# Optimization experiments

Hardware: AMD Instinct MI355X
Metric: run time of the kernel (lower is better)

## Reference

```python
import jax, jax.numpy as jnp
import numpy as np

BATCH, TOK, DIM, OUT = 4, 2048, 4096, 4096
E, R, TOP_K = 8, 16, 2
SCALING = 16.0 / R  # lora_alpha / r


def setup_inputs() -> dict:
    key = jax.random.key(0)
    ks = jax.random.split(key, 6)
    return {
        "x": jax.random.normal(ks[0], (BATCH, TOK, DIM), dtype=jnp.float32),
        "W_base": jax.random.normal(ks[1], (OUT, DIM), dtype=jnp.float32) / np.sqrt(DIM),
        "b_base": jax.random.normal(ks[2], (OUT,), dtype=jnp.float32) * 0.01,
        "W_gate": jax.random.normal(ks[3], (E, DIM), dtype=jnp.float32) * 0.01,
        "A": jax.random.normal(ks[4], (E, R, DIM), dtype=jnp.float32) / np.sqrt(DIM),
        "B": jax.random.normal(ks[5], (OUT, OUT // OUT * R * 0 + R), dtype=jnp.float32)[None].repeat(E, 0) * 0.0 + jax.random.normal(ks[5], (E, OUT, R), dtype=jnp.float32) * 0.02,
    }


def reference(x, W_base, b_base, W_gate, A, B):
    # Base frozen linear: [B,N,D] @ [D,O] -> [B,N,O]
    result = jnp.einsum("bnd,od->bno", x, W_base) + b_base
    # Gating
    logits = jnp.einsum("bnd,ed->bne", x, W_gate)
    probs = jax.nn.softmax(logits.astype(jnp.float32), axis=-1)  # fp32 softmax
    top_p, top_i = jax.lax.top_k(probs, TOP_K)  # [B,N,K]
    top_p = top_p / jnp.sum(top_p, axis=-1, keepdims=True)  # top_k > 1 branch
    top_p = top_p.astype(x.dtype)
    # Scatter top-k probs back to dense [B,N,E] routing weights
    route_w = jnp.sum(jax.nn.one_hot(top_i, E, dtype=x.dtype) * top_p[..., None], axis=-2)
    # Per-expert LoRA: down-project all tokens for all experts (r is small),
    # weight by routing, then up-project and sum over experts.
    h = jnp.einsum("bnd,erd->bner", x, A)          # [B,N,E,r]
    hw = h * route_w[..., None]                      # mask/combine weighting
    delta = jnp.einsum("bner,eor->bno", hw, B)      # [B,N,O]
    return result + delta * SCALING
```

## Files before the change

### kernel.cpp

```cpp
#include <hip/hip_runtime.h>
#include <hip/hip_bf16.h>
#include <cstdint>

#define TOKENS 8192
#define DIM_   4096
#define OUTD   4096
#define NE     8
#define NR     16
#define LORA_COLS (NE*NR)
#define KCAT  (DIM_ + LORA_COLS)
#define NTILES (KCAT/64)

typedef __attribute__((ext_vector_type(8))) short short8;
typedef __attribute__((ext_vector_type(4))) float f32x4;

__device__ __forceinline__ unsigned short f2bf(float f) {
  union { float f; unsigned u; } v; v.f = f;
  unsigned r = v.u + 0x7FFFu + ((v.u >> 16) & 1u);
  return (unsigned short)(r >> 16);
}

__device__ __forceinline__ void load_lds16(const void* g, void* l) {
  auto gp = reinterpret_cast<const __attribute__((address_space(1))) unsigned int*>(
      reinterpret_cast<uintptr_t>(g));
  auto lp = reinterpret_cast<__attribute__((address_space(3))) unsigned int*>(
      reinterpret_cast<uintptr_t>(l));
  __builtin_amdgcn_global_load_lds(gp, lp, 16, 0, 0);
}

#define BAR() asm volatile("s_barrier" ::: "memory")
#define LGKM0() do { asm volatile("s_waitcnt lgkmcnt(0)" ::: "memory"); \
                     __builtin_amdgcn_sched_barrier(0); } while (0)
#define VMW(N) asm volatile("s_waitcnt vmcnt(" #N ")" ::: "memory")

__global__ __launch_bounds__(256) void conv_w_kernel(
    const float* __restrict__ W, const float* __restrict__ Bm,
    const float* __restrict__ Am, unsigned short* __restrict__ Wcat,
    unsigned short* __restrict__ Acat, float scaling) {
  int b = blockIdx.x, tid = threadIdx.x;
  if (b < OUTD) {
    const float4* src = (const float4*)(W + (size_t)b * DIM_);
    unsigned short* dst = Wcat + (size_t)b * KCAT;
#pragma unroll
    for (int j = 0; j < DIM_ / 1024; ++j) {
      float4 v = src[j * 256 + tid];
      ushort4 o; o.x = f2bf(v.x); o.y = f2bf(v.y); o.z = f2bf(v.z); o.w = f2bf(v.w);
      *(ushort4*)(dst + (size_t)(j * 256 + tid) * 4) = o;
    }
    if (tid < LORA_COLS) {
      int e = tid >> 4, r = tid & 15;
      dst[DIM_ + tid] = f2bf(scaling * Bm[((size_t)e * OUTD + b) * NR + r]);
    }
  } else {
    int i = b - OUTD;
    const float4* src = (const float4*)(Am + (size_t)i * DIM_);
    unsigned short* dst = Acat + (size_t)i * DIM_;
#pragma unroll
    for (int j = 0; j < DIM_ / 1024; ++j) {
      float4 v = src[j * 256 + tid];
      ushort4 o; o.x = f2bf(v.x); o.y = f2bf(v.y); o.z = f2bf(v.z); o.w = f2bf(v.w);
      *(ushort4*)(dst + (size_t)(j * 256 + tid) * 4) = o;
    }
  }
}

__global__ __launch_bounds__(256) void prep_x_kernel(
    const float* __restrict__ x, const float* __restrict__ Wg,
    unsigned short* __restrict__ Xcat, int* __restrict__ ridx,
    float* __restrict__ rw) {
  __shared__ float red[32 * 257];
  __shared__ float lg[32];
  int tid = threadIdx.x;
  int t0 = blockIdx.x * 4;
  float acc[4][8];
#pragma unroll
  for (int ti = 0; ti < 4; ++ti)
#pragma unroll
    for (int e = 0; e < 8; ++e) acc[ti][e] = 0.f;
  const float4* x4 = (const float4*)x;
  const float4* wg4 = (const float4*)Wg;
#pragma unroll
  for (int j = 0; j < 4; ++j) {
    int dpos = j * 256 + tid;
    float4 wg[8];
#pragma unroll
    for (int e = 0; e < 8; ++e) wg[e] = wg4[e * 1024 + dpos];
#pragma unroll
    for (int ti = 0; ti < 4; ++ti) {
      float4 v = x4[(size_t)(t0 + ti) * 1024 + dpos];
      ushort4 o; o.x = f2bf(v.x); o.y = f2bf(v.y); o.z = f2bf(v.z); o.w = f2bf(v.w);
      *(ushort4*)&Xcat[(size_t)(t0 + ti) * KCAT + (size_t)dpos * 4] = o;
#pragma unroll
      for (int e = 0; e < 8; ++e)
        acc[ti][e] += v.x * wg[e].x + v.y * wg[e].y + v.z * wg[e].z + v.w * wg[e].w;
    }
  }
#pragma unroll
  for (int p = 0; p < 32; ++p) red[p * 257 + tid] = acc[p >> 3][p & 7];
  __syncthreads();
  {
    int p = tid >> 3, part = tid & 7;
    float s = 0.f;
#pragma unroll
    for (int i = 0; i < 32; ++i) s += red[p * 257 + part * 32 + i];
    s += __shfl_xor(s, 1);
    s += __shfl_xor(s, 2);
    s += __shfl_xor(s, 4);
    if (part == 0) lg[p] = s;
  }
  __syncthreads();
  if (tid < 4) {
    float l[8];
#pragma unroll
    for (int e = 0; e < 8; ++e) l[e] = lg[tid * 8 + e];
    int i0 = 0; float m0 = l[0];
#pragma unroll
    for (int e = 1; e < 8; ++e) if (l[e] > m0) { m0 = l[e]; i0 = e; }
    int i1 = -1; float m1 = -3.4e38f;
#pragma unroll
    for (int e = 0; e < 8; ++e) if (e != i0 && l[e] > m1) { m1 = l[e]; i1 = e; }
    float w0 = 1.0f / (1.0f + expf(m1 - m0));
    int t = t0 + tid;
    ridx[t * 2] = i0; ridx[t * 2 + 1] = i1;
    rw[t * 2] = w0;  rw[t * 2 + 1] = 1.0f - w0;
  }
}

template <int MODE>
__global__ __launch_bounds__(256) void gemm_kernel(
    const unsigned short* __restrict__ Aop, const unsigned short* __restrict__ Bop,
    float* __restrict__ Cout, unsigned short* __restrict__ CoutBf,
    const float* __restrict__ bias, const int* __restrict__ ridx,
    const float* __restrict__ rw,
    int M, int N, int K, int lda, int ldb, int ldc) {
  __shared__ __align__(16) unsigned short lsA[128 * 32];
  __shared__ __align__(16) unsigned short lsB[128 * 32];
  int tid = threadIdx.x;
  int lane = tid & 63, wave = tid >> 6;
  int wm = wave >> 1, wn = wave & 1;
  int row0 = blockIdx.x * 128, col0 = blockIdx.y * 128;

  f32x4 acc[4][4];
#pragma unroll
  for (int a = 0; a < 4; ++a)
#pragma unroll
    for (int b = 0; b < 4; ++b) acc[a][b] = (f32x4){0.f, 0.f, 0.f, 0.f};

  int lrow = lane >> 2;
  int lcol = (lane & 3) << 3;
  int fr = lane & 15, fk = (lane >> 4) << 3;

  const unsigned short* gA0 = Aop + (size_t)(row0 + wave * 32 + lrow) * lda + lcol;
  const unsigned short* gA1 = Aop + (size_t)(row0 + wave * 32 + 16 + lrow) * lda + lcol;
  const unsigned short* gB0 = Bop + (size_t)(col0 + wave * 32 + lrow) * ldb + lcol;
  const unsigned short* gB1 = Bop + (size_t)(col0 + wave * 32 + 16 + lrow) * ldb + lcol;

  for (int k0 = 0; k0 < K; k0 += 32) {
    load_lds16(gA0 + k0, lsA + wave * 1024);
    load_lds16(gA1 + k0, lsA + wave * 1024 + 512);
    load_lds16(gB0 + k0, lsB + wave * 1024);
    load_lds16(gB1 + k0, lsB + wave * 1024 + 512);
    __syncthreads();
    short8 af[4], bfr[4];
#pragma unroll
    for (int mi = 0; mi < 4; ++mi)
      af[mi] = *(const short8*)&lsA[(wm * 64 + mi * 16 + fr) * 32 + fk];
#pragma unroll
    for (int ni = 0; ni < 4; ++ni)
      bfr[ni] = *(const short8*)&lsB[(wn * 64 + ni * 16 + fr) * 32 + fk];
#pragma unroll
    for (int mi = 0; mi < 4; ++mi)
#pragma unroll
      for (int ni = 0; ni < 4; ++ni)
        acc[mi][ni] = __builtin_amdgcn_mfma_f32_16x16x32_bf16(af[mi], bfr[ni], acc[mi][ni], 0, 0, 0);
    __syncthreads();
  }

  int fg = lane >> 4;
  if (MODE == 0) {
#pragma unroll
    for (int ni = 0; ni < 4; ++ni) {
      int col = col0 + wn * 64 + ni * 16 + fr;
      float bv = bias[col];
#pragma unroll
      for (int mi = 0; mi < 4; ++mi)
#pragma unroll
        for (int j = 0; j < 4; ++j) {
          int row = row0 + wm * 64 + mi * 16 + fg * 4 + j;
          Cout[(size_t)row * ldc + col] = acc[mi][ni][j] + bv;
        }
    }
  } else {
#pragma unroll
    for (int mi = 0; mi < 4; ++mi)
#pragma unroll
      for (int j = 0; j < 4; ++j) {
        int row = row0 + wm * 64 + mi * 16 + fg * 4 + j;
        int i0 = ridx[row * 2], i1 = ridx[row * 2 + 1];
        float w0 = rw[row * 2], w1 = rw[row * 2 + 1];
#pragma unroll
        for (int ni = 0; ni < 4; ++ni) {
          int col = wn * 64 + ni * 16 + fr;
          int e = col >> 4;
          float w = (e == i0) ? w0 : ((e == i1) ? w1 : 0.f);
          CoutBf[(size_t)row * ldc + col] = f2bf(w * acc[mi][ni][j]);
        }
      }
  }
}

#define RD_A4(dst, base, ks, mi0) do { \
  dst[0] = *(const short8*)((base) + (((mi0)+0)*2+(ks))*1024); \
  dst[1] = *(const short8*)((base) + (((mi0)+1)*2+(ks))*1024); \
  dst[2] = *(const short8*)((base) + (((mi0)+2)*2+(ks))*1024); \
  dst[3] = *(const short8*)((base) + (((mi0)+3)*2+(ks))*1024); } while (0)
#define RD_B4(dst, base, ks) do { \
  dst[0] = *(const short8*)((base) + 0*2048 + (ks)*1024); \
  dst[1] = *(const short8*)((base) + 1*2048 + (ks)*1024); \
  dst[2] = *(const short8*)((base) + 2*2048 + (ks)*1024); \
  dst[3] = *(const short8*)((base) + 3*2048 + (ks)*1024); } while (0)
#define MFMA_BLK(a4, b4, m0) do { \
  __builtin_amdgcn_s_setprio(1); \
  _Pragma("unroll") \
  for (int mi = 0; mi < 4; ++mi) { \
    _Pragma("unroll") \
    for (int ni = 0; ni < 4; ++ni) { \
      acc[(m0)+mi][ni] = __builtin_amdgcn_mfma_f32_16x16x32_bf16( \
          a4[mi], b4[ni], acc[(m0)+mi][ni], 0, 0, 0); } } \
  __builtin_amdgcn_s_setprio(0); } while (0)
#define STAGE(srcp, kofs, dst) do { \
  load_lds16((srcp) + (kofs), (dst)); \
  load_lds16((srcp) + (kofs) + 32, (dst) + 1024); } while (0)

__global__ __launch_bounds__(512, 2) void gemm256_kernel(
    const unsigned short* __restrict__ Aop,
    const unsigned short* __restrict__ Bop,
    float* __restrict__ Cout, const float* __restrict__ bias) {
  extern __shared__ char lds[];
  const int tid = threadIdx.x;
  const int lane = tid & 63, wave = tid >> 6;
  const int wm = wave >> 2, wn = wave & 3;
  const int fr = lane & 15, kg = lane >> 4;

  const int bid = blockIdx.x;
  const int swz = (bid & 7) * 64 + (bid >> 3);
  const int mt = swz >> 4, nt = swz & 15;
  const int row0 = mt * 256, col0 = nt * 256;

  const int srow = lane >> 2;
  const int scol = ((lane & 3) * 8) ^ (((lane >> 5) & 1) * 16);
  const unsigned short* sA0 = Aop + (size_t)(row0 +       wave * 16 + srow) * KCAT + scol;
  const unsigned short* sA1 = Aop + (size_t)(row0 + 128 + wave * 16 + srow) * KCAT + scol;
  const unsigned short* sB0 = Bop + (size_t)(col0 +       wave * 16 + srow) * KCAT + scol;
  const unsigned short* sB1 = Bop + (size_t)(col0 + 128 + wave * 16 + srow) * KCAT + scol;

  char* dA0b0 = lds +      0 + wave * 2048;
  char* dA1b0 = lds +  16384 + wave * 2048;
  char* dB0b0 = lds +  32768 + wave * 2048;
  char* dB1b0 = lds +  49152 + wave * 2048;
  char* dA0b1 = dA0b0 + 65536;
  char* dA1b1 = dA1b0 + 65536;
  char* dB0b1 = dB0b0 + 65536;
  char* dB1b1 = dB1b0 + 65536;

  const int swzo = (kg * 16) ^ ((fr >> 3) << 5);
  const char* rdA0 = lds + wm * 16384 + fr * 64 + swzo;
  const char* rdA1 = rdA0 + 65536;
  const char* rdB0 = lds + 32768 + (wn >> 1) * 16384 + (wn & 1) * 8192 + fr * 64 + swzo;
  const char* rdB1 = rdB0 + 65536;

  f32x4 acc[8][4];
#pragma unroll
  for (int a = 0; a < 8; ++a)
#pragma unroll
    for (int b = 0; b < 4; ++b) acc[a][b] = (f32x4){0.f, 0.f, 0.f, 0.f};

  STAGE(sA0, 0, dA0b0); STAGE(sA1, 0, dA1b0);
  STAGE(sB0, 0, dB0b0); STAGE(sB1, 0, dB1b0);
  STAGE(sB0, 64, dB0b1); STAGE(sA0, 64, dA0b1);
  VMW(4);
  BAR();

  for (int i = 0; i < NTILES / 2 - 1; ++i) {
    const int k1 = (2 * i + 1) * 64, k2 = k1 + 64, k3 = k1 + 128;
    short8 aL[4], aH[4], a1L[4], a1H[4], b0f[4], b1f[4];
    RD_A4(aL, rdA0, 0, 0); RD_B4(b0f, rdB0, 0);
    STAGE(sB1, k1, dB1b1);
    BAR(); LGKM0();
    MFMA_BLK(aL, b0f, 0);
    BAR();
    RD_A4(aH, rdA0, 0, 4); RD_B4(b1f, rdB0, 1);
    STAGE(sA1, k1, dA1b1);
    BAR(); LGKM0();
    MFMA_BLK(aH, b0f, 4);
    BAR();
    RD_A4(a1L, rdA0, 1, 0); RD_A4(a1H, rdA0, 1, 4);
    STAGE(sB0, k2, dB0b0);
    BAR(); LGKM0();
    MFMA_BLK(a1L, b1f, 0);
    BAR();
    STAGE(sA0, k2, dA0b0);
    BAR();
    MFMA_BLK(a1H, b1f, 4);
    VMW(4);
    BAR();
    RD_A4(aL, rdA1, 0, 0); RD_B4(b0f, rdB1, 0);
    STAGE(sB1, k2, dB1b0);
    BAR(); LGKM0();
    MFMA_BLK(aL, b0f, 0);
    BAR();
    RD_A4(aH, rdA1, 0, 4); RD_B4(b1f, rdB1, 1);
    STAGE(sA1, k2, dA1b0);
    BAR(); LGKM0();
    MFMA_BLK(aH, b0f, 4);
    BAR();
    RD_A4(a1L, rdA1, 1, 0); RD_A4(a1H, rdA1, 1, 4);
    STAGE(sB0, k3, dB0b1);
    BAR(); LGKM0();
    MFMA_BLK(a1L, b1f, 0);
    BAR();
    STAGE(sA0, k3, dA0b1);
    BAR();
    MFMA_BLK(a1H, b1f, 4);
    VMW(4);
    BAR();
  }

  {
    const int k65 = 65 * 64;
    short8 aL[4], aH[4], a1L[4], a1H[4], b0f[4], b1f[4];
    RD_A4(aL, rdA0, 0, 0); RD_B4(b0f, rdB0, 0);
    STAGE(sB1, k65, dB1b1);
    BAR(); LGKM0();
    MFMA_BLK(aL, b0f, 0);
    BAR();
    RD_A4(aH, rdA0, 0, 4); RD_B4(b1f, rdB0, 1);
    STAGE(sA1, k65, dA1b1);
    BAR(); LGKM0();
    MFMA_BLK(aH, b0f, 4);
    BAR();
    RD_A4(a1L, rdA0, 1, 0); RD_A4(a1H, rdA0, 1, 4);
    BAR(); LGKM0();
    MFMA_BLK(a1L, b1f, 0);
    BAR();
    MFMA_BLK(a1H, b1f, 4);
    VMW(0);
    BAR();
    RD_A4(aL, rdA1, 0, 0); RD_B4(b0f, rdB1, 0); RD_A4(aH, rdA1, 0, 4);
    LGKM0();
    MFMA_BLK(aL, b0f, 0);
    MFMA_BLK(aH, b0f, 4);
    RD_A4(a1L, rdA1, 1, 0); RD_B4(b1f, rdB1, 1); RD_A4(a1H, rdA1, 1, 4);
    LGKM0();
    MFMA_BLK(a1L, b1f, 0);
    MFMA_BLK(a1H, b1f, 4);
  }

#pragma unroll
  for (int ni = 0; ni < 4; ++ni) {
    int col = col0 + wn * 64 + ni * 16 + fr;
    float bv = bias[col];
#pragma unroll
    for (int mi = 0; mi < 8; ++mi)
#pragma unroll
      for (int j = 0; j < 4; ++j) {
        int row = row0 + wm * 128 + mi * 16 + kg * 4 + j;
        Cout[(size_t)row * OUTD + col] = acc[mi][ni][j] + bv;
      }
  }
}

extern "C" void kernel_launch(void* const* d_in, const int* in_sizes, int n_in,
                              void* d_out, int out_size, void* d_ws, size_t ws_size,
                              hipStream_t stream) {
  const float* x  = (const float*)d_in[0];
  const float* Wb = (const float*)d_in[1];
  const float* bb = (const float*)d_in[2];
  const float* Wg = (const float*)d_in[3];
  const float* Am = (const float*)d_in[4];
  const float* Bm = (const float*)d_in[5];
  float* out = (float*)d_out;

  unsigned short* Wcat = (unsigned short*)d_ws;
  unsigned short* Xcat = Wcat + (size_t)OUTD * KCAT;
  unsigned short* Acat = Xcat + (size_t)TOKENS * KCAT;
  int*   ridx = (int*)(Acat + (size_t)LORA_COLS * DIM_);
  float* rw   = (float*)(ridx + (size_t)TOKENS * 2);

  const float scaling = 16.0f / (float)NR;

  hipFuncSetAttribute((const void*)gemm256_kernel,
                      hipFuncAttributeMaxDynamicSharedMemorySize, 131072);

  conv_w_kernel<<<dim3(OUTD + LORA_COLS), dim3(256), 0, stream>>>(
      Wb, Bm, Am, Wcat, Acat, scaling);
  prep_x_kernel<<<dim3(TOKENS / 4), dim3(256), 0, stream>>>(
      x, Wg, Xcat, ridx, rw);
  gemm_kernel<1><<<dim3(TOKENS / 128, 1), dim3(256), 0, stream>>>(
      Xcat, Acat, (float*)nullptr, Xcat + DIM_, (const float*)nullptr,
      ridx, rw, TOKENS, LORA_COLS, DIM_, KCAT, DIM_, KCAT);
  gemm256_kernel<<<dim3(512), dim3(512), 131072, stream>>>(Xcat, Wcat, out, bb);
}
```

Measured before the change: 377.8 us.

## Split-K the LoRA down-projection GEMM and vectorize main GEMM epilogue stores

The LoRA down-projection (tokens x 128 x 4096) previously ran on only 64 blocks. It is now split over K into 8 slices writing fp32 partials, followed by a combine kernel that sums them, applies routing weights and writes bf16 into Xcat. This path is only taken if the workspace is large enough. Separately, the main GEMM swaps the MFMA operand order so each lane holds 4 consecutive columns, which lets the epilogue use float4 stores and a float4 bias load. The cost is extra partial-buffer traffic and one more kernel launch, and the workspace-size check may leave the new path unused.

```diff
diff --git a/kernel.cpp b/kernel.cpp
--- a/kernel.cpp
+++ b/kernel.cpp
@@ -10,6 +10,8 @@
 #define LORA_COLS (NE*NR)
 #define KCAT  (DIM_ + LORA_COLS)
 #define NTILES (KCAT/64)
+#define HSPLIT 8
+#define HKC    (DIM_/HSPLIT)
 
 typedef __attribute__((ext_vector_type(8))) short short8;
 typedef __attribute__((ext_vector_type(4))) float f32x4;
@@ -207,6 +209,84 @@
         }
       }
   }
+}
+
+__global__ __launch_bounds__(256) void gemm_h_sk_kernel(
+    const unsigned short* __restrict__ Aop,
+    const unsigned short* __restrict__ Bop,
+    float* __restrict__ Hpart) {
+  __shared__ __align__(16) unsigned short lsA[128 * 32];
+  __shared__ __align__(16) unsigned short lsB[128 * 32];
+  int tid = threadIdx.x;
+  int lane = tid & 63, wave = tid >> 6;
+  int wm = wave >> 1, wn = wave & 1;
+  int row0 = blockIdx.x * 128;
+  int s = blockIdx.y;
+  int kbeg = s * HKC;
+
+  f32x4 acc[4][4];
+#pragma unroll
+  for (int a = 0; a < 4; ++a)
+#pragma unroll
+    for (int b = 0; b < 4; ++b) acc[a][b] = (f32x4){0.f, 0.f, 0.f, 0.f};
+
+  int lrow = lane >> 2;
+  int lcol = (lane & 3) << 3;
+  int fr = lane & 15, fk = (lane >> 4) << 3;
+
+  const unsigned short* gA0 = Aop + (size_t)(row0 + wave * 32 + lrow) * KCAT + lcol;
+  const unsigned short* gA1 = Aop + (size_t)(row0 + wave * 32 + 16 + lrow) * KCAT + lcol;
+  const unsigned short* gB0 = Bop + (size_t)(wave * 32 + lrow) * DIM_ + lcol;
+  const unsigned short* gB1 = Bop + (size_t)(wave * 32 + 16 + lrow) * DIM_ + lcol;
+
+  for (int k0 = kbeg; k0 < kbeg + HKC; k0 += 32) {
+    load_lds16(gA0 + k0, lsA + wave * 1024);
+    load_lds16(gA1 + k0, lsA + wave * 1024 + 512);
+    load_lds16(gB0 + k0, lsB + wave * 1024);
+    load_lds16(gB1 + k0, lsB + wave * 1024 + 512);
+    __syncthreads();
+    short8 af[4], bfr[4];
+#pragma unroll
+    for (int mi = 0; mi < 4; ++mi)
+      af[mi] = *(const short8*)&lsA[(wm * 64 + mi * 16 + fr) * 32 + fk];
+#pragma unroll
+    for (int ni = 0; ni < 4; ++ni)
+      bfr[ni] = *(const short8*)&lsB[(wn * 64 + ni * 16 + fr) * 32 + fk];
+#pragma unroll
+    for (int mi = 0; mi < 4; ++mi)
+#pragma unroll
+      for (int ni = 0; ni < 4; ++ni)
+        acc[mi][ni] = __builtin_amdgcn_mfma_f32_16x16x32_bf16(af[mi], bfr[ni], acc[mi][ni], 0, 0, 0);
+    __syncthreads();
+  }
+
+  int fg = lane >> 4;
+  float* outp = Hpart + (size_t)s * TOKENS * 128;
+#pragma unroll
+  for (int ni = 0; ni < 4; ++ni) {
+    int col = wn * 64 + ni * 16 + fr;
+#pragma unroll
+    for (int mi = 0; mi < 4; ++mi)
+#pragma unroll
+      for (int j = 0; j < 4; ++j) {
+        int row = row0 + wm * 64 + mi * 16 + fg * 4 + j;
+        outp[(size_t)row * 128 + col] = acc[mi][ni][j];
+      }
+  }
+}
+
+__global__ __launch_bounds__(256) void h_combine_kernel(
+    const float* __restrict__ Hpart, const int* __restrict__ ridx,
+    const float* __restrict__ rw, unsigned short* __restrict__ Xcat) {
+  int gid = blockIdx.x * 256 + threadIdx.x;
+  int t = gid >> 7, c = gid & 127;
+  float s = 0.f;
+#pragma unroll
+  for (int i = 0; i < HSPLIT; ++i) s += Hpart[(size_t)i * TOKENS * 128 + gid];
+  int e = c >> 4;
+  int i0 = ridx[t * 2], i1 = ridx[t * 2 + 1];
+  float w = (e == i0) ? rw[t * 2] : ((e == i1) ? rw[t * 2 + 1] : 0.f);
+  Xcat[(size_t)t * KCAT + DIM_ + c] = f2bf(w * s);
 }
 
 #define RD_A4(dst, base, ks, mi0) do { \
@@ -226,7 +306,7 @@
     _Pragma("unroll") \
     for (int ni = 0; ni < 4; ++ni) { \
       acc[(m0)+mi][ni] = __builtin_amdgcn_mfma_f32_16x16x32_bf16( \
-          a4[mi], b4[ni], acc[(m0)+mi][ni], 0, 0, 0); } } \
+          b4[ni], a4[mi], acc[(m0)+mi][ni], 0, 0, 0); } } \
   __builtin_amdgcn_s_setprio(0); } while (0)
 #define STAGE(srcp, kofs, dst) do { \
   load_lds16((srcp) + (kofs), (dst)); \
@@ -358,15 +438,18 @@
 
 #pragma unroll
   for (int ni = 0; ni < 4; ++ni) {
-    int col = col0 + wn * 64 + ni * 16 + fr;
-    float bv = bias[col];
-#pragma unroll
-    for (int mi = 0; mi < 8; ++mi)
-#pragma unroll
-      for (int j = 0; j < 4; ++j) {
-        int row = row0 + wm * 128 + mi * 16 + kg * 4 + j;
-        Cout[(size_t)row * OUTD + col] = acc[mi][ni][j] + bv;
-      }
+    int colb = col0 + wn * 64 + ni * 16 + kg * 4;
+    float4 bv = *(const float4*)&bias[colb];
+#pragma unroll
+    for (int mi = 0; mi < 8; ++mi) {
+      int row = row0 + wm * 128 + mi * 16 + fr;
+      float4 v;
+      v.x = acc[mi][ni][0] + bv.x;
+      v.y = acc[mi][ni][1] + bv.y;
+      v.z = acc[mi][ni][2] + bv.z;
+      v.w = acc[mi][ni][3] + bv.w;
+      *(float4*)&Cout[(size_t)row * OUTD + colb] = v;
+    }
   }
 }
 
@@ -386,6 +469,11 @@
   unsigned short* Acat = Xcat + (size_t)TOKENS * KCAT;
   int*   ridx = (int*)(Acat + (size_t)LORA_COLS * DIM_);
   float* rw   = (float*)(ridx + (size_t)TOKENS * 2);
+  float* Hpart = (float*)(rw + (size_t)TOKENS * 2);
+
+  const size_t ws_needed = (size_t)((char*)(Hpart + (size_t)HSPLIT * TOKENS * 128)
+                                    - (char*)d_ws);
+  const bool use_splitk = (ws_size >= ws_needed);
 
   const float scaling = 16.0f / (float)NR;
 
@@ -396,8 +484,15 @@
       Wb, Bm, Am, Wcat, Acat, scaling);
   prep_x_kernel<<<dim3(TOKENS / 4), dim3(256), 0, stream>>>(
       x, Wg, Xcat, ridx, rw);
-  gemm_kernel<1><<<dim3(TOKENS / 128, 1), dim3(256), 0, stream>>>(
-      Xcat, Acat, (float*)nullptr, Xcat + DIM_, (const float*)nullptr,
-      ridx, rw, TOKENS, LORA_COLS, DIM_, KCAT, DIM_, KCAT);
+  if (use_splitk) {
+    gemm_h_sk_kernel<<<dim3(TOKENS / 128, HSPLIT), dim3(256), 0, stream>>>(
+        Xcat, Acat, Hpart);
+    h_combine_kernel<<<dim3(TOKENS * 128 / 256), dim3(256), 0, stream>>>(
+        Hpart, ridx, rw, Xcat);
+  } else {
+    gemm_kernel<1><<<dim3(TOKENS / 128, 1), dim3(256), 0, stream>>>(
+        Xcat, Acat, (float*)nullptr, Xcat + DIM_, (const float*)nullptr,
+        ridx, rw, TOKENS, LORA_COLS, DIM_, KCAT, DIM_, KCAT);
+  }
   gemm256_kernel<<<dim3(512), dim3(512), 131072, stream>>>(Xcat, Wcat, out, bb);
 }
```

New measurement: 323.9 us. -14.3%, faster.
